# Performance work log

Hardware: AMD Instinct MI355X
Metric: run time of the kernel (lower is better)

## Reference

```python
import jax, jax.numpy as jnp
import numpy as np

B, C, H, W = 4, 512, 64, 64
C8 = C // 8
BN_EPS = 1e-5


def setup_inputs() -> dict:
    key = jax.random.key(0)
    ks = jax.random.split(key, 9)
    x = jax.random.normal(ks[0], (B, C, H, W), jnp.float32)
    # 1x1 convs are channel-mixing matrices (out_ch, in_ch), no bias
    wq = 0.02 * jax.random.normal(ks[1], (C8, C), jnp.float32)
    wk = 0.02 * jax.random.normal(ks[2], (C8, C), jnp.float32)
    wv = 0.02 * jax.random.normal(ks[3], (C, C), jnp.float32)
    w_fuse = 0.02 * jax.random.normal(ks[4], (C, C), jnp.float32)
    # gammas init to 0 in the module; use small random values so the
    # attention branches actually contribute to outputs/grads
    gamma_pa = 0.5 + 0.1 * jax.random.normal(ks[5], (1,), jnp.float32)
    gamma_ca = 0.5 + 0.1 * jax.random.normal(ks[6], (1,), jnp.float32)
    bn_scale = 1.0 + 0.1 * jax.random.normal(ks[7], (C,), jnp.float32)
    bn_bias = 0.1 * jax.random.normal(ks[8], (C,), jnp.float32)
    return {"x": x, "wq": wq, "wk": wk, "wv": wv, "w_fuse": w_fuse,
            "gamma_pa": gamma_pa, "gamma_ca": gamma_ca,
            "bn_scale": bn_scale, "bn_bias": bn_bias}


def reference(x, wq, wk, wv, w_fuse, gamma_pa, gamma_ca, bn_scale, bn_bias):
    b, c, h, w = x.shape
    n = h * w
    xf = x.reshape(b, c, n)                         # [B, C, N]

    # ---- Position attention (over N = H*W spatial positions) ----
    q = jnp.einsum('oc,bcn->bon', wq, xf)           # [B, C/8, N]
    k = jnp.einsum('oc,bcn->bon', wk, xf)           # [B, C/8, N]
    v = jnp.einsum('oc,bcn->bon', wv, xf)           # [B, C, N]
    energy = jnp.einsum('bcn,bcm->bnm', q, k)       # [B, N, N] (no scaling, as in source)
    attn = jax.nn.softmax(energy, axis=-1)
    # out = v @ attn^T  ->  out[b,c,n] = sum_m v[b,c,m] * attn[b,n,m]
    pa = jnp.einsum('bcm,bnm->bcn', v, attn).reshape(b, c, h, w)
    pa = gamma_pa * pa + x

    # ---- Channel attention (over C channels, max-subtracted variant) ----
    ce = jnp.einsum('bcn,bdn->bcd', xf, xf)         # [B, C, C]
    ce = jnp.max(ce, axis=-1, keepdims=True) - ce
    cattn = jax.nn.softmax(ce, axis=-1)
    ca = jnp.einsum('bcd,bdn->bcn', cattn, xf).reshape(b, c, h, w)
    ca = gamma_ca * ca + x

    # ---- Fuse: 1x1 conv -> BatchNorm (training-mode batch stats) -> ReLU ----
    s = pa + ca
    y = jnp.einsum('oc,bchw->bohw', w_fuse, s)
    mean = jnp.mean(y, axis=(0, 2, 3), keepdims=True)
    var = jnp.var(y, axis=(0, 2, 3), keepdims=True)
    y = (y - mean) * jax.lax.rsqrt(var + BN_EPS)
    y = y * bn_scale.reshape(1, -1, 1, 1) + bn_bias.reshape(1, -1, 1, 1)
    return jax.nn.relu(y)
```

## Files before the change

kernel.cpp:

```cpp
#include <hip/hip_runtime.h>
#include <cstdint>
#include <cstddef>

#define B_   4
#define C_   512
#define N_   4096
#define BN_EPS 1e-5f

typedef __attribute__((ext_vector_type(8))) short short8;
typedef __attribute__((ext_vector_type(8))) unsigned short ushort8;
typedef __attribute__((ext_vector_type(4))) unsigned short us4_t;
typedef __attribute__((ext_vector_type(4))) float f32x4;

__device__ __forceinline__ unsigned short f2b(float f) {
  union { float f; unsigned u; } v; v.f = f;
  unsigned u = v.u;
  return (unsigned short)((u + 0x7fffu + ((u >> 16) & 1u)) >> 16);
}
__device__ __forceinline__ float b2f(unsigned short h) {
  union { unsigned u; float f; } v; v.u = ((unsigned)h) << 16;
  return v.f;
}
__device__ __forceinline__ void async16(const void* g, void* l) {
  __builtin_amdgcn_global_load_lds((const __attribute__((address_space(1))) void*)g,
                                   (__attribute__((address_space(3))) void*)l, 16, 0, 0);
}


__global__ __launch_bounds__(256) void convert_x_k(const float* __restrict__ x,
                                                   unsigned short* __restrict__ xcn,
                                                   unsigned short* __restrict__ xnc,
                                                   const float* __restrict__ wq,
                                                   const float* __restrict__ wk,
                                                   const float* __restrict__ wv,
                                                   const float* __restrict__ wf,
                                                   unsigned short* __restrict__ wqk,
                                                   unsigned short* __restrict__ wvb,
                                                   unsigned short* __restrict__ wfb) {
  __shared__ float tile[64][65];
  int bz = blockIdx.z;
  if (bz == 4) {
    int lin = (blockIdx.y * 8 + blockIdx.x) * 256 + threadIdx.x;
    wvb[lin] = f2b(wv[lin]);  wvb[lin + 131072] = f2b(wv[lin + 131072]);
    wfb[lin] = f2b(wf[lin]);  wfb[lin + 131072] = f2b(wf[lin + 131072]);
    if (lin < 65536) {
      int row = lin >> 9, col = lin & 511;
      float v = (row < 64) ? wq[row * 512 + col] : wk[(row - 64) * 512 + col];
      wqk[lin] = f2b(v);
    }
    return;
  }
  int c0 = blockIdx.x * 64, n0 = blockIdx.y * 64, b = bz;
  const float* xb = x + ((size_t)b * C_ + c0) * N_ + n0;
  unsigned short* cn = xcn + ((size_t)b * C_ + c0) * N_ + n0;
#pragma unroll
  for (int j = 0; j < 16; ++j) {
    int lin = j * 256 + threadIdx.x;
    int rr = lin >> 6, cc = lin & 63;
    float v = xb[(size_t)rr * N_ + cc];
    cn[(size_t)rr * N_ + cc] = f2b(v);
    tile[cc][rr] = v;
  }
  __syncthreads();
  unsigned short* nc = xnc + ((size_t)b * N_ + n0) * C_ + c0;
#pragma unroll
  for (int j = 0; j < 16; ++j) {
    int lin = j * 256 + threadIdx.x;
    int rr = lin >> 6, cc = lin & 63;
    nc[(size_t)rr * C_ + cc] = f2b(tile[rr][cc]);
  }
}


enum { EPI_BF16 = 0, EPI_F32 = 1, EPI_YB = 2 };

template<int EPI, bool SPLITK>
__device__ __forceinline__ void gemm_core(
    const unsigned short* __restrict__ A, size_t lda, size_t sA,
    const unsigned short* __restrict__ Bm, size_t ldb, size_t sB,
    void* __restrict__ Cv, size_t ldc, size_t sCbytes, int K,
    float* __restrict__ part, int bx, int by, int bz,
    unsigned short* lsA, unsigned short* lsB) {
  const int m0 = bx * 128, n0 = by * 128;
  char* Cb;
  if (SPLITK) {
    int bidx = bz & 3, ch = bz >> 2;
    A  += (size_t)bidx * sA + (size_t)ch * (size_t)K;
    Bm += (size_t)bidx * sB + (size_t)ch * (size_t)K;
    Cb = (char*)Cv + (size_t)bidx * sCbytes + (size_t)ch * 4u * sCbytes;
  } else {
    A  += (size_t)bz * sA;
    Bm += (size_t)bz * sB;
    Cb = (char*)Cv + (size_t)bz * sCbytes;
  }
  const int tid = threadIdx.x, lane = tid & 63, w = tid >> 6;
  const int wm = (w >> 1) * 64, wn = (w & 1) * 64;
  const int fr = lane & 15, fk = (lane >> 4) * 8;
  f32x4 acc[4][4];
#pragma unroll
  for (int i = 0; i < 4; ++i)
#pragma unroll
    for (int j = 0; j < 4; ++j) acc[i][j] = (f32x4){0.f, 0.f, 0.f, 0.f};

  const int i0 = tid, i1 = tid + 256;
  for (int k0 = 0; k0 < K; k0 += 32) {
    async16(A  + (size_t)(m0 + (i0 >> 2)) * lda + k0 + (i0 & 3) * 8, (char*)lsA + i0 * 16);
    async16(A  + (size_t)(m0 + (i1 >> 2)) * lda + k0 + (i1 & 3) * 8, (char*)lsA + i1 * 16);
    async16(Bm + (size_t)(n0 + (i0 >> 2)) * ldb + k0 + (i0 & 3) * 8, (char*)lsB + i0 * 16);
    async16(Bm + (size_t)(n0 + (i1 >> 2)) * ldb + k0 + (i1 & 3) * 8, (char*)lsB + i1 * 16);
    __syncthreads();
    short8 af[4], bfr[4];
#pragma unroll
    for (int mi = 0; mi < 4; ++mi)
      af[mi] = *(const short8*)&lsA[(wm + mi * 16 + fr) * 32 + fk];
#pragma unroll
    for (int ni = 0; ni < 4; ++ni)
      bfr[ni] = *(const short8*)&lsB[(wn + ni * 16 + fr) * 32 + fk];
#pragma unroll
    for (int mi = 0; mi < 4; ++mi)
#pragma unroll
      for (int ni = 0; ni < 4; ++ni)
        acc[mi][ni] = __builtin_amdgcn_mfma_f32_16x16x32_bf16(af[mi], bfr[ni], acc[mi][ni], 0, 0, 0);
    __syncthreads();
  }
  float cs[4] = {0.f, 0.f, 0.f, 0.f}, cq[4] = {0.f, 0.f, 0.f, 0.f};
#pragma unroll
  for (int mi = 0; mi < 4; ++mi)
#pragma unroll
    for (int ni = 0; ni < 4; ++ni)
#pragma unroll
      for (int r = 0; r < 4; ++r) {
        int gr = m0 + wm + mi * 16 + (lane >> 4) * 4 + r;
        int gc = n0 + wn + ni * 16 + fr;
        float v = acc[mi][ni][r];
        if (EPI == EPI_F32) ((float*)Cb)[(size_t)gr * ldc + gc] = v;
        else                ((unsigned short*)Cb)[(size_t)gr * ldc + gc] = f2b(v);
        if (EPI == EPI_YB) { cs[ni] += v; cq[ni] += v * v; }
      }
  if (EPI == EPI_YB) {
#pragma unroll
    for (int ni = 0; ni < 4; ++ni) {
      cs[ni] += __shfl_xor(cs[ni], 16, 64); cs[ni] += __shfl_xor(cs[ni], 32, 64);
      cq[ni] += __shfl_xor(cq[ni], 16, 64); cq[ni] += __shfl_xor(cq[ni], 32, 64);
    }
    float* fb = (float*)lsA;
    if (lane < 16) {
#pragma unroll
      for (int ni = 0; ni < 4; ++ni) {
        int col = wn + ni * 16 + lane;
        fb[((w >> 1) * 128 + col) * 2]     = cs[ni];
        fb[((w >> 1) * 128 + col) * 2 + 1] = cq[ni];
      }
    }
    __syncthreads();
    if (tid < 128) {
      float s = fb[tid * 2] + fb[(128 + tid) * 2];
      float q = fb[tid * 2 + 1] + fb[(128 + tid) * 2 + 1];
      int rg = bz * 32 + bx;
      int gcol = by * 128 + tid;
      part[(size_t)rg * 1024 + gcol * 2]     = s;
      part[(size_t)rg * 1024 + gcol * 2 + 1] = q;
    }
  }
}

template<int EPI, bool SPLITK = false>
__global__ __launch_bounds__(256)
void gemm_bt(const unsigned short* __restrict__ A, size_t lda, size_t sA,
             const unsigned short* __restrict__ Bm, size_t ldb, size_t sB,
             void* __restrict__ Cv, size_t ldc, size_t sCbytes, int K,
             float* __restrict__ part) {
  __shared__ unsigned short lsA[128 * 32];
  __shared__ unsigned short lsB[128 * 32];
  gemm_core<EPI, SPLITK>(A, lda, sA, Bm, ldb, sB, Cv, ldc, sCbytes, K, part,
                         blockIdx.x, blockIdx.y, blockIdx.z, lsA, lsB);
}

__global__ __launch_bounds__(256)
void gemm3_k(const unsigned short* __restrict__ xnc, const unsigned short* __restrict__ xcn,
             const unsigned short* __restrict__ wqkb, const unsigned short* __restrict__ wvb,
             unsigned short* __restrict__ qkT, unsigned short* __restrict__ vmat,
             float* __restrict__ cepart) {
  __shared__ unsigned short lsA[128 * 32];
  __shared__ unsigned short lsB[128 * 32];
  int id = blockIdx.x;
  if (id < 256) {
    gemm_core<EPI_F32, true>(xcn, N_, (size_t)C_ * N_, xcn, N_, (size_t)C_ * N_,
                             cepart, 512, (size_t)512 * 512 * 4, 1024, nullptr,
                             id & 3, (id >> 2) & 3, id >> 4, lsA, lsB);
  } else if (id < 384) {
    int t = id - 256;
    gemm_core<EPI_BF16, false>(xnc, 512, (size_t)N_ * C_, wqkb, 512, 0,
                               qkT, 128, (size_t)N_ * 128 * 2, 512, nullptr,
                               t & 31, 0, t >> 5, lsA, lsB);
  } else {
    int t = id - 384;
    gemm_core<EPI_BF16, false>(wvb, 512, 0, xnc, 512, (size_t)N_ * C_,
                               vmat, N_, (size_t)C_ * N_ * 2, 512, nullptr,
                               t & 3, (t >> 2) & 31, t >> 7, lsA, lsB);
  }
}

#define QR 128
#define CC 256
#define KT 128

__global__ __launch_bounds__(512, 2)
void fused_pa_k(const unsigned short* __restrict__ qkT,
                const unsigned short* __restrict__ vmat,
                const unsigned short* __restrict__ caT,
                const unsigned short* __restrict__ xnc,
                const float* __restrict__ gpa_p, const float* __restrict__ gca_p,
                unsigned short* __restrict__ sT) {
  __shared__ unsigned short lsQ[QR * 64];
  __shared__ unsigned short lsK[2][KT * 64];
  __shared__ unsigned short lsV[CC * KT];
  __shared__ unsigned short lsP[QR * KT];
  __shared__ float lsL[8][64];
  __shared__ float invL[QR];

  const int bid = blockIdx.x;
  const int combo = bid & 7;
  const int b = combo >> 1, chalf = combo & 1;
  const int qt = bid >> 3;
  const int n0 = qt * QR, c0 = chalf * CC;

  const int tid = threadIdx.x, lane = tid & 63, w = tid >> 6;
  const int fr = lane & 15, fq = lane >> 4;
  const int wr = w >> 2, wc = w & 3;
  const int ms = (w & 3) * 32;
  const int nb = (w >> 2) * 64;

  const unsigned short* qk_b = qkT + (size_t)b * N_ * 128;
  const unsigned short* v_b  = vmat + (size_t)b * C_ * N_;

  f32x4 acc[4][4];
#pragma unroll
  for (int i = 0; i < 4; ++i)
#pragma unroll
    for (int j = 0; j < 4; ++j) acc[i][j] = (f32x4){0.f, 0.f, 0.f, 0.f};
  float lsum[4] = {0.f, 0.f, 0.f, 0.f};

#pragma unroll
  for (int j = 0; j < 2; ++j) {
    int idx = j * 512 + tid;
    int r = idx >> 3, g = idx & 7;
    async16(qk_b + (size_t)(n0 + r) * 128 + ((g ^ (r & 7)) << 3), (char*)lsQ + idx * 16);
  }
#pragma unroll
  for (int j = 0; j < 2; ++j) {
    int idx = j * 512 + tid;
    int r = idx >> 3, g = idx & 7;
    async16(qk_b + (size_t)r * 128 + 64 + ((g ^ (r & 7)) << 3), (char*)lsK[0] + idx * 16);
  }
  __syncthreads();

  for (int it = 0; it < N_ / KT; ++it) {
    const int m0 = it * KT;
#pragma unroll
    for (int j = 0; j < 8; ++j) {
      int idx = j * 512 + tid;
      int c = idx >> 4, g = idx & 15;
      async16(v_b + (size_t)(c0 + c) * N_ + m0 + ((g ^ (c & 7)) << 3), (char*)lsV + idx * 16);
    }
    if (it < N_ / KT - 1) {
      unsigned short* dst = lsK[(it + 1) & 1];
#pragma unroll
      for (int j = 0; j < 2; ++j) {
        int idx = j * 512 + tid;
        int r = idx >> 3, g = idx & 7;
        async16(qk_b + (size_t)(m0 + KT + r) * 128 + 64 + ((g ^ (r & 7)) << 3),
                (char*)dst + idx * 16);
      }
    }
    const unsigned short* lk = lsK[it & 1];
    short8 afk[2][2];
#pragma unroll
    for (int mi = 0; mi < 2; ++mi)
#pragma unroll
      for (int kk = 0; kk < 2; ++kk)
        afk[mi][kk] = *(const short8*)&lk[(ms + mi * 16 + fr) * 64 + (((kk * 4 + fq) ^ (fr & 7)) << 3)];
#pragma unroll
    for (int f = 0; f < 4; ++f) {
      int n = nb + f * 16 + fr;
      short8 bq0 = *(const short8*)&lsQ[n * 64 + (((0 * 4 + fq) ^ (fr & 7)) << 3)];
      short8 bq1 = *(const short8*)&lsQ[n * 64 + (((1 * 4 + fq) ^ (fr & 7)) << 3)];
      float part = 0.f;
#pragma unroll
      for (int mi = 0; mi < 2; ++mi) {
        f32x4 e = (f32x4){0.f, 0.f, 0.f, 0.f};
        e = __builtin_amdgcn_mfma_f32_16x16x32_bf16(afk[mi][0], bq0, e, 0, 0, 0);
        e = __builtin_amdgcn_mfma_f32_16x16x32_bf16(afk[mi][1], bq1, e, 0, 0, 0);
        float p0 = __expf(e[0]), p1 = __expf(e[1]), p2 = __expf(e[2]), p3 = __expf(e[3]);
        part += (p0 + p1) + (p2 + p3);
        int mb = ms + mi * 16 + fq * 4;
        us4_t pk = { f2b(p0), f2b(p1), f2b(p2), f2b(p3) };
        *(us4_t*)((char*)lsP + n * 256 + ((((mb >> 3) ^ (n & 7)) << 3) + (mb & 7)) * 2) = pk;
      }
      part += __shfl_xor(part, 16, 64);
      part += __shfl_xor(part, 32, 64);
      lsum[f] += part;
    }
    __syncthreads();
#pragma unroll
    for (int kk4 = 0; kk4 < 4; ++kk4) {
      short8 pa[4], vbf[4];
#pragma unroll
      for (int mi = 0; mi < 4; ++mi) {
        int n = wr * 64 + mi * 16 + fr;
        pa[mi] = *(const short8*)((const char*)lsP + n * 256 + (((kk4 * 4 + fq) ^ (n & 7)) << 4));
      }
#pragma unroll
      for (int ni = 0; ni < 4; ++ni) {
        int c = wc * 64 + ni * 16 + fr;
        vbf[ni] = *(const short8*)((const char*)lsV + c * 256 + (((kk4 * 4 + fq) ^ (c & 7)) << 4));
      }
#pragma unroll
      for (int mi = 0; mi < 4; ++mi)
#pragma unroll
        for (int ni = 0; ni < 4; ++ni)
          acc[mi][ni] = __builtin_amdgcn_mfma_f32_16x16x32_bf16(pa[mi], vbf[ni], acc[mi][ni], 0, 0, 0);
    }
    __syncthreads();
  }

  if (lane < 16) {
#pragma unroll
    for (int f = 0; f < 4; ++f) lsL[w][f * 16 + lane] = lsum[f];
  }
  __syncthreads();
  if (tid < QR) {
    int nh = tid >> 6, j = tid & 63;
    invL[tid] = 1.f / (lsL[4 * nh][j] + lsL[4 * nh + 1][j] + lsL[4 * nh + 2][j] + lsL[4 * nh + 3][j]);
  }
  __syncthreads();

  const float gpa = gpa_p[0], gca = gca_p[0];
#pragma unroll
  for (int mi = 0; mi < 4; ++mi)
#pragma unroll
    for (int ni = 0; ni < 4; ++ni)
#pragma unroll
      for (int r = 0; r < 4; ++r) {
        int nl = wr * 64 + mi * 16 + fq * 4 + r;
        int gn = n0 + nl;
        int gc = c0 + wc * 64 + ni * 16 + fr;
        size_t eo = ((size_t)b * N_ + gn) * C_ + gc;
        float sv = gpa * acc[mi][ni][r] * invL[nl] + gca * b2f(caT[eo]) + 2.f * b2f(xnc[eo]);
        sT[eo] = f2b(sv);
      }
}

__global__ __launch_bounds__(256) void ce_softmax_k(const float* __restrict__ cepart,
                                                    unsigned short* __restrict__ cattn) {
  int wid = threadIdx.x >> 6, lane = threadIdx.x & 63;
  size_t row = (size_t)blockIdx.x * 4 + wid;
  float v[8]; float mn = 3.4e38f;
#pragma unroll
  for (int i = 0; i < 8; ++i) {
    size_t idx = row * C_ + (size_t)(i * 64 + lane);
    float t = cepart[idx] + cepart[idx + 1048576] + cepart[idx + 2097152] + cepart[idx + 3145728];
    v[i] = t; mn = fminf(mn, t);
  }
#pragma unroll
  for (int o = 1; o < 64; o <<= 1) mn = fminf(mn, __shfl_xor(mn, o, 64));
  float s = 0.f, p[8];
#pragma unroll
  for (int i = 0; i < 8; ++i) { p[i] = expf(mn - v[i]); s += p[i]; }
#pragma unroll
  for (int o = 1; o < 64; o <<= 1) s += __shfl_xor(s, o, 64);
  float inv = 1.f / s;
  unsigned short* orow = cattn + row * C_;
#pragma unroll
  for (int i = 0; i < 8; ++i) orow[i * 64 + lane] = f2b(p[i] * inv);
}

__global__ __launch_bounds__(256) void bn_apply_k(const unsigned short* __restrict__ yT,
                                                  const float* __restrict__ part,
                                                  const float* __restrict__ bns,
                                                  const float* __restrict__ bnb,
                                                  float* __restrict__ out) {
  __shared__ float tile[64][65];
  __shared__ float red[4][64][2];
  __shared__ float abv[64][2];
  int n0 = blockIdx.x * 64, o0 = blockIdx.y * 64, b = blockIdx.z;
  int t = threadIdx.x;
  {
    int col = o0 + (t & 63), seg = t >> 6;
    float s = 0.f, q = 0.f;
    for (int p = seg * 32; p < seg * 32 + 32; ++p) {
      s += part[(size_t)p * 1024 + col * 2];
      q += part[(size_t)p * 1024 + col * 2 + 1];
    }
    red[seg][t & 63][0] = s; red[seg][t & 63][1] = q;
  }
  __syncthreads();
  if (t < 64) {
    float S = red[0][t][0] + red[1][t][0] + red[2][t][0] + red[3][t][0];
    float Q = red[0][t][1] + red[1][t][1] + red[2][t][1] + red[3][t][1];
    float mean = S * (1.f / 16384.f);
    float var  = Q * (1.f / 16384.f) - mean * mean;
    float istd = rsqrtf(var + BN_EPS);
    float a = bns[o0 + t] * istd;
    abv[t][0] = a;
    abv[t][1] = bnb[o0 + t] - mean * a;
  }
  __syncthreads();
  const unsigned short* yb = yT + ((size_t)b * N_ + n0) * C_ + o0;
#pragma unroll
  for (int j = 0; j < 16; ++j) {
    int lin = j * 256 + t;
    int rr = lin >> 6, cc = lin & 63;
    float v = b2f(yb[(size_t)rr * C_ + cc]);
    tile[cc][rr] = fmaxf(v * abv[cc][0] + abv[cc][1], 0.f);
  }
  __syncthreads();
  float* ob = out + ((size_t)b * C_ + o0) * N_ + n0;
#pragma unroll
  for (int j = 0; j < 16; ++j) {
    int lin = j * 256 + t;
    int rr = lin >> 6, cc = lin & 63;
    ob[(size_t)rr * N_ + cc] = tile[rr][cc];
  }
}


extern "C" void kernel_launch(void* const* d_in, const int* in_sizes, int n_in,
                              void* d_out, int out_size, void* d_ws, size_t ws_size,
                              hipStream_t stream) {
  (void)in_sizes; (void)n_in; (void)out_size; (void)ws_size;
  const float* x   = (const float*)d_in[0];
  const float* wq  = (const float*)d_in[1];
  const float* wk  = (const float*)d_in[2];
  const float* wv  = (const float*)d_in[3];
  const float* wf  = (const float*)d_in[4];
  const float* gpa = (const float*)d_in[5];
  const float* gca = (const float*)d_in[6];
  const float* bns = (const float*)d_in[7];
  const float* bnb = (const float*)d_in[8];
  float* out = (float*)d_out;

  char* ws = (char*)d_ws;
  size_t off = 0;
  auto carve = [&](size_t bytes) -> char* {
    off = (off + 255) & ~(size_t)255;
    char* p = ws + off; off += bytes; return p;
  };

  unsigned short* xcn   = (unsigned short*)carve((size_t)B_ * C_ * N_ * 2);
  unsigned short* xnc   = (unsigned short*)carve((size_t)B_ * C_ * N_ * 2);
  unsigned short* wqkb  = (unsigned short*)carve(128 * 512 * 2);
  unsigned short* wvb   = (unsigned short*)carve(512 * 512 * 2);
  unsigned short* wfb   = (unsigned short*)carve(512 * 512 * 2);
  unsigned short* qkT   = (unsigned short*)carve((size_t)B_ * N_ * 128 * 2);
  unsigned short* vmat  = (unsigned short*)carve((size_t)B_ * C_ * N_ * 2);
  float*          cepart= (float*)carve((size_t)4 * B_ * 512 * 512 * 4);
  unsigned short* cattn = (unsigned short*)carve((size_t)B_ * 512 * 512 * 2);
  unsigned short* caT   = (unsigned short*)carve((size_t)B_ * N_ * C_ * 2);
  float*          bnpart= (float*)carve((size_t)128 * 1024 * 4);

  unsigned short* yT = (unsigned short*)cepart;
  unsigned short* sT = xcn;

  convert_x_k<<<dim3(C_ / 64, N_ / 64, 5), 256, 0, stream>>>(
      x, xcn, xnc, wq, wk, wv, wf, wqkb, wvb, wfb);

  gemm3_k<<<dim3(896), 256, 0, stream>>>(xnc, xcn, wqkb, wvb, qkT, vmat, cepart);

  ce_softmax_k<<<dim3(B_ * 512 / 4), 256, 0, stream>>>(cepart, cattn);

  gemm_bt<EPI_BF16><<<dim3(32, 4, 4), 256, 0, stream>>>(
      xnc, 512, (size_t)N_ * C_, cattn, 512, (size_t)512 * 512,
      caT, 512, (size_t)N_ * C_ * 2, 512, nullptr);

  fused_pa_k<<<dim3(256), 512, 0, stream>>>(qkT, vmat, caT, xnc, gpa, gca, sT);

  gemm_bt<EPI_YB><<<dim3(32, 4, 4), 256, 0, stream>>>(
      sT, 512, (size_t)N_ * C_, wfb, 512, 0,
      yT, 512, (size_t)N_ * C_ * 2, 512, bnpart);

  bn_apply_k<<<dim3(N_ / 64, C_ / 64, B_), 256, 0, stream>>>(yT, bnpart, bns, bnb, out);
}
```

Measured before the change: 214.7 us.

## Fuse channel-attention GEMM into position-attention kernel epilogue

Removes the separate gemm_bt launch that produced the caT channel-attention output and instead computes cattn·x inside fused_pa_k. After the PV loop, the accumulators are pre-scaled by gamma_pa/L, and four extra MFMA blocks then accumulate the x·cattn^T product through the existing LDS tiles. Gamma_ca is folded into the softmax normalization. This avoids writing and re-reading a B×N×C bf16 intermediate and one kernel launch. The cost is a longer tail per block with synchronous staging and no double buffering.

```diff
diff --git a/kernel.cpp b/kernel.cpp
--- a/kernel.cpp
+++ b/kernel.cpp
@@ -208,9 +208,9 @@
 __global__ __launch_bounds__(512, 2)
 void fused_pa_k(const unsigned short* __restrict__ qkT,
                 const unsigned short* __restrict__ vmat,
-                const unsigned short* __restrict__ caT,
+                const unsigned short* __restrict__ cattn,
                 const unsigned short* __restrict__ xnc,
-                const float* __restrict__ gpa_p, const float* __restrict__ gca_p,
+                const float* __restrict__ gpa_p,
                 unsigned short* __restrict__ sT) {
   __shared__ unsigned short lsQ[QR * 64];
   __shared__ unsigned short lsK[2][KT * 64];
@@ -233,6 +233,8 @@
 
   const unsigned short* qk_b = qkT + (size_t)b * N_ * 128;
   const unsigned short* v_b  = vmat + (size_t)b * C_ * N_;
+  const unsigned short* xn_b = xnc + (size_t)b * N_ * C_;
+  const unsigned short* ct_b = cattn + (size_t)b * 512 * 512;
 
   f32x4 acc[4][4];
 #pragma unroll
@@ -240,6 +242,44 @@
 #pragma unroll
     for (int j = 0; j < 4; ++j) acc[i][j] = (f32x4){0.f, 0.f, 0.f, 0.f};
   float lsum[4] = {0.f, 0.f, 0.f, 0.f};
+
+  auto pvblock = [&]() {
+#pragma unroll
+    for (int kk4 = 0; kk4 < 4; ++kk4) {
+      short8 pa[4], vbf[4];
+#pragma unroll
+      for (int mi = 0; mi < 4; ++mi) {
+        int n = wr * 64 + mi * 16 + fr;
+        pa[mi] = *(const short8*)((const char*)lsP + n * 256 + (((kk4 * 4 + fq) ^ (n & 7)) << 4));
+      }
+#pragma unroll
+      for (int ni = 0; ni < 4; ++ni) {
+        int c = wc * 64 + ni * 16 + fr;
+        vbf[ni] = *(const short8*)((const char*)lsV + c * 256 + (((kk4 * 4 + fq) ^ (c & 7)) << 4));
+      }
+#pragma unroll
+      for (int mi = 0; mi < 4; ++mi)
+#pragma unroll
+        for (int ni = 0; ni < 4; ++ni)
+          acc[mi][ni] = __builtin_amdgcn_mfma_f32_16x16x32_bf16(pa[mi], vbf[ni], acc[mi][ni], 0, 0, 0);
+    }
+  };
+  auto stage_ca = [&](int d0) {
+#pragma unroll
+    for (int j = 0; j < 4; ++j) {
+      int idx = j * 512 + tid;
+      int r = idx >> 4, g = idx & 15;
+      async16(xn_b + (size_t)(n0 + r) * C_ + d0 * 128 + ((g ^ (r & 7)) << 3),
+              (char*)lsP + idx * 16);
+    }
+#pragma unroll
+    for (int j = 0; j < 8; ++j) {
+      int idx = j * 512 + tid;
+      int c = idx >> 4, g = idx & 15;
+      async16(ct_b + (size_t)(c0 + c) * 512 + d0 * 128 + ((g ^ (c & 7)) << 3),
+              (char*)lsV + idx * 16);
+    }
+  };
 
 #pragma unroll
   for (int j = 0; j < 2; ++j) {
@@ -302,27 +342,11 @@
       lsum[f] += part;
     }
     __syncthreads();
-#pragma unroll
-    for (int kk4 = 0; kk4 < 4; ++kk4) {
-      short8 pa[4], vbf[4];
-#pragma unroll
-      for (int mi = 0; mi < 4; ++mi) {
-        int n = wr * 64 + mi * 16 + fr;
-        pa[mi] = *(const short8*)((const char*)lsP + n * 256 + (((kk4 * 4 + fq) ^ (n & 7)) << 4));
-      }
-#pragma unroll
-      for (int ni = 0; ni < 4; ++ni) {
-        int c = wc * 64 + ni * 16 + fr;
-        vbf[ni] = *(const short8*)((const char*)lsV + c * 256 + (((kk4 * 4 + fq) ^ (c & 7)) << 4));
-      }
-#pragma unroll
-      for (int mi = 0; mi < 4; ++mi)
-#pragma unroll
-        for (int ni = 0; ni < 4; ++ni)
-          acc[mi][ni] = __builtin_amdgcn_mfma_f32_16x16x32_bf16(pa[mi], vbf[ni], acc[mi][ni], 0, 0, 0);
-    }
+    pvblock();
     __syncthreads();
   }
+
+  stage_ca(0);
 
   if (lane < 16) {
 #pragma unroll
@@ -335,7 +359,25 @@
   }
   __syncthreads();
 
-  const float gpa = gpa_p[0], gca = gca_p[0];
+  const float gpa = gpa_p[0];
+#pragma unroll
+  for (int mi = 0; mi < 4; ++mi)
+#pragma unroll
+    for (int r = 0; r < 4; ++r) {
+      float sc = gpa * invL[wr * 64 + mi * 16 + fq * 4 + r];
+#pragma unroll
+      for (int ni = 0; ni < 4; ++ni) acc[mi][ni][r] *= sc;
+    }
+
+  for (int d0 = 0; d0 < 4; ++d0) {
+    pvblock();
+    if (d0 < 3) {
+      __syncthreads();
+      stage_ca(d0 + 1);
+      __syncthreads();
+    }
+  }
+
 #pragma unroll
   for (int mi = 0; mi < 4; ++mi)
 #pragma unroll
@@ -346,12 +388,13 @@
         int gn = n0 + nl;
         int gc = c0 + wc * 64 + ni * 16 + fr;
         size_t eo = ((size_t)b * N_ + gn) * C_ + gc;
-        float sv = gpa * acc[mi][ni][r] * invL[nl] + gca * b2f(caT[eo]) + 2.f * b2f(xnc[eo]);
+        float sv = acc[mi][ni][r] + 2.f * b2f(xnc[eo]);
         sT[eo] = f2b(sv);
       }
 }
 
 __global__ __launch_bounds__(256) void ce_softmax_k(const float* __restrict__ cepart,
+                                                    const float* __restrict__ gca_p,
                                                     unsigned short* __restrict__ cattn) {
   int wid = threadIdx.x >> 6, lane = threadIdx.x & 63;
   size_t row = (size_t)blockIdx.x * 4 + wid;
@@ -369,7 +412,7 @@
   for (int i = 0; i < 8; ++i) { p[i] = expf(mn - v[i]); s += p[i]; }
 #pragma unroll
   for (int o = 1; o < 64; o <<= 1) s += __shfl_xor(s, o, 64);
-  float inv = 1.f / s;
+  float inv = gca_p[0] / s;
   unsigned short* orow = cattn + row * C_;
 #pragma unroll
   for (int i = 0; i < 8; ++i) orow[i * 64 + lane] = f2b(p[i] * inv);
@@ -456,7 +499,6 @@
   unsigned short* vmat  = (unsigned short*)carve((size_t)B_ * C_ * N_ * 2);
   float*          cepart= (float*)carve((size_t)4 * B_ * 512 * 512 * 4);
   unsigned short* cattn = (unsigned short*)carve((size_t)B_ * 512 * 512 * 2);
-  unsigned short* caT   = (unsigned short*)carve((size_t)B_ * N_ * C_ * 2);
   float*          bnpart= (float*)carve((size_t)128 * 1024 * 4);
 
   unsigned short* yT = (unsigned short*)cepart;
@@ -467,13 +509,9 @@
 
   gemm3_k<<<dim3(896), 256, 0, stream>>>(xnc, xcn, wqkb, wvb, qkT, vmat, cepart);
 
-  ce_softmax_k<<<dim3(B_ * 512 / 4), 256, 0, stream>>>(cepart, cattn);
-
-  gemm_bt<EPI_BF16><<<dim3(32, 4, 4), 256, 0, stream>>>(
-      xnc, 512, (size_t)N_ * C_, cattn, 512, (size_t)512 * 512,
-      caT, 512, (size_t)N_ * C_ * 2, 512, nullptr);
-
-  fused_pa_k<<<dim3(256), 512, 0, stream>>>(qkT, vmat, caT, xnc, gpa, gca, sT);
+  ce_softmax_k<<<dim3(B_ * 512 / 4), 256, 0, stream>>>(cepart, gca, cattn);
+
+  fused_pa_k<<<dim3(256), 512, 0, stream>>>(qkT, vmat, cattn, xnc, gpa, sT);
 
   gemm_bt<EPI_YB><<<dim3(32, 4, 4), 256, 0, stream>>>(
       sT, 512, (size_t)N_ * C_, wfb, 512, 0,
```

Measured after the change: 225.0 us. +4.8%, slower.
